# Kernel optimization log

Measured on AMD Instinct MI355X. Metric: run time of the kernel, lower is better.

The kernel has to match this reference:

```python
import jax, jax.numpy as jnp
import numpy as np

B, S, E, H = 2, 2048, 1024, 16
DH = E // H  # 64


def setup_inputs() -> dict:
    key = jax.random.key(0)
    ks = jax.random.split(key, 13)
    s = 1.0 / np.sqrt(E)
    inp = {
        'query': jax.random.normal(ks[0], (B, S, E), jnp.float32),
        'key':   jax.random.normal(ks[1], (B, S, E), jnp.float32),
        'value': jax.random.normal(ks[2], (B, S, E), jnp.float32),
        # nn.Linear weights stored [out, in]
        'Wq': jax.random.uniform(ks[3], (E, E), jnp.float32, -s, s),
        'bq': jax.random.uniform(ks[4], (E,), jnp.float32, -s, s),
        'Wk': jax.random.uniform(ks[5], (E, E), jnp.float32, -s, s),
        'bk': jax.random.uniform(ks[6], (E,), jnp.float32, -s, s),
        'Wv': jax.random.uniform(ks[7], (E, E), jnp.float32, -s, s),
        'bv': jax.random.uniform(ks[8], (E,), jnp.float32, -s, s),
        # 1x1 Conv2d over head channels: weight [H, H] (squeezed from [H,H,1,1]), bias [H]
        'Wc': jax.random.uniform(ks[9], (H, H), jnp.float32, -1.0 / np.sqrt(H), 1.0 / np.sqrt(H)),
        'bc': jax.random.uniform(ks[10], (H,), jnp.float32, -1.0 / np.sqrt(H), 1.0 / np.sqrt(H)),
        'Wo': jax.random.uniform(ks[11], (E, E), jnp.float32, -s, s),
        'bo': jax.random.uniform(ks[12], (E,), jnp.float32, -s, s),
    }
    return inp


def reference(query, key, value, Wq, bq, Wk, bk, Wv, bv, Wc, bc, Wo, bo):
    b, s = query.shape[0], query.shape[1]
    # projections -> (B, H, S, Dh)
    def split_heads(x):
        return x.reshape(b, s, H, DH).transpose(0, 2, 1, 3)
    Q = split_heads(query @ Wq.T + bq)
    K = split_heads(key @ Wk.T + bk)
    V = split_heads(value @ Wv.T + bv)
    # raw scores (B, H, S, S)
    scores = jnp.einsum('bhqd,bhkd->bhqk', Q, K) / np.sqrt(DH).astype(np.float32)
    # 1x1 conv mixes logits across heads: channel-wise matmul + bias
    noise = jnp.einsum('gh,bhqk->bgqk', Wc, scores) + bc[None, :, None, None]
    scores = scores + noise
    weights = jax.nn.softmax(scores, axis=-1)
    out = jnp.einsum('bhqk,bhkd->bhqd', weights, V)  # (B, H, S, Dh)
    out = out.transpose(0, 2, 1, 3).reshape(b, s, E)
    return out @ Wo.T + bo
```

## Files before the change

### kernel.cpp

```cpp
#include <hip/hip_runtime.h>


typedef __attribute__((ext_vector_type(8))) short bf16x8_t;
typedef __attribute__((ext_vector_type(4))) short bf16x4_t;
typedef __attribute__((ext_vector_type(4))) float f32x4_t;

__device__ inline unsigned short f2bf(float f) {
  unsigned u = __builtin_bit_cast(unsigned, f);
  u += 0x7fffu + ((u >> 16) & 1u);
  return (unsigned short)(u >> 16);
}

struct ConvArgs {
  const float* src[7];
  unsigned short* dst[7];
  int n[7];
};

__global__ __launch_bounds__(256) void convert_f32_bf16(ConvArgs a) {
  const int which = blockIdx.y;
  const int i = (blockIdx.x * 256 + threadIdx.x) * 8;
  if (i >= a.n[which]) return;
  const float* s = a.src[which] + i;
  f32x4_t x0 = *(const f32x4_t*)(s);
  f32x4_t x1 = *(const f32x4_t*)(s + 4);
  bf16x8_t o;
#pragma unroll
  for (int j = 0; j < 4; j++) o[j] = (short)f2bf(x0[j]);
#pragma unroll
  for (int j = 0; j < 4; j++) o[4 + j] = (short)f2bf(x1[j]);
  *(bf16x8_t*)(a.dst[which] + i) = o;
}

__global__ __launch_bounds__(256) void gemm_bt(
    const unsigned short* __restrict__ A, const unsigned short* __restrict__ Bt,
    const float* __restrict__ bias, void* __restrict__ C,
    int M, int N, int K, int c_is_f32)
{
  __shared__ unsigned short As[128 * 32];
  __shared__ unsigned short Bs[128 * 32];
  const int t = threadIdx.x;
  const int l = t & 63;
  const int w = t >> 6;
  const int quad = l >> 4, n16 = l & 15;
  const int wm = (w & 1) * 64, wn = (w >> 1) * 64;
  const long m0 = (long)blockIdx.x * 128, n0 = (long)blockIdx.y * 128;

  f32x4_t acc[4][4] = {};

  const unsigned short* gA = A + (m0 + (t >> 2)) * (long)K + (t & 3) * 8;
  const unsigned short* gB = Bt + (n0 + (t >> 2)) * (long)K + (t & 3) * 8;
  const long rowskip = 64l * K;

  for (int kt = 0; kt < K; kt += 32) {
    bf16x8_t ra0 = *(const bf16x8_t*)(gA + kt);
    bf16x8_t ra1 = *(const bf16x8_t*)(gA + kt + rowskip);
    bf16x8_t rb0 = *(const bf16x8_t*)(gB + kt);
    bf16x8_t rb1 = *(const bf16x8_t*)(gB + kt + rowskip);
    __syncthreads();
    *(bf16x8_t*)&As[t * 8] = ra0;
    *(bf16x8_t*)&As[2048 + t * 8] = ra1;
    *(bf16x8_t*)&Bs[t * 8] = rb0;
    *(bf16x8_t*)&Bs[2048 + t * 8] = rb1;
    __syncthreads();
    bf16x8_t af[4], bfr[4];
#pragma unroll
    for (int i = 0; i < 4; i++) {
      af[i]  = *(const bf16x8_t*)&As[(wm + i * 16 + n16) * 32 + quad * 8];
      bfr[i] = *(const bf16x8_t*)&Bs[(wn + i * 16 + n16) * 32 + quad * 8];
    }
#pragma unroll
    for (int mi = 0; mi < 4; mi++)
#pragma unroll
      for (int ni = 0; ni < 4; ni++)
        acc[mi][ni] = __builtin_amdgcn_mfma_f32_16x16x32_bf16(af[mi], bfr[ni], acc[mi][ni], 0, 0, 0);
  }

#pragma unroll
  for (int ni = 0; ni < 4; ni++) {
    const long n = n0 + wn + ni * 16 + n16;
    const float bv = bias[n];
#pragma unroll
    for (int mi = 0; mi < 4; mi++) {
#pragma unroll
      for (int r = 0; r < 4; r++) {
        const long m = m0 + wm + mi * 16 + quad * 4 + r;
        const float v = acc[mi][ni][r] + bv;
        if (c_is_f32) ((float*)C)[m * N + n] = v;
        else ((unsigned short*)C)[m * N + n] = f2bf(v);
      }
    }
  }
}

__global__ __launch_bounds__(256) void transpose_v(
    const unsigned short* __restrict__ V, unsigned short* __restrict__ VT)
{
  __shared__ unsigned short tile[64][72];
  const int t = threadIdx.x;
  const int s0 = blockIdx.x * 64, h = blockIdx.y, b = blockIdx.z;
#pragma unroll
  for (int r = 0; r < 2; r++) {
    const int elem = r * 2048 + t * 8;
    const int s = elem >> 6, d = elem & 63;
    *(bf16x8_t*)&tile[s][d] =
        *(const bf16x8_t*)&V[(size_t)(b * 2048 + s0 + s) * 1024 + h * 64 + d];
  }
  __syncthreads();
#pragma unroll
  for (int r = 0; r < 2; r++) {
    const int elem = r * 2048 + t * 8;
    const int d = elem >> 6, sl = elem & 63;
    bf16x8_t o;
#pragma unroll
    for (int j = 0; j < 8; j++) o[j] = (short)tile[sl + j][d];
    *(bf16x8_t*)&VT[((size_t)(b * 16 + h) * 64 + d) * 2048 + s0 + sl] = o;
  }
}

__global__ __launch_bounds__(1024) void attention_fused(
    const unsigned short* __restrict__ Qb, const unsigned short* __restrict__ Kb,
    const unsigned short* __restrict__ VT, const float* __restrict__ Wc,
    unsigned short* __restrict__ Obuf)
{
  __shared__ unsigned short sraw[512 * 36];
  __shared__ unsigned short pbuf2[16 * 580];
  __shared__ float alphabuf[256];
  __shared__ float lbuf[256];
  __shared__ unsigned short mmat[256];

  const int t = threadIdx.x;
  const int g = t >> 6, l = t & 63;
  const int quad = l >> 4, n16 = l & 15;

  const int id = blockIdx.x;
  const int xcd = id & 7;
  const int b = xcd >> 2;
  const int qb = (xcd & 3) * 32 + (id >> 3);
  const int q0 = qb * 16;

  if (t < 256) {
    const float v = ((((t >> 4) == (t & 15)) ? 1.0f : 0.0f) + Wc[t]) * 0.125f;
    mmat[t] = f2bf(v);
  }
  __syncthreads();

  bf16x8_t mfrag;
  if (quad < 2) mfrag = *(const bf16x8_t*)&mmat[n16 * 16 + quad * 8];
  else { bf16x8_t z = {0, 0, 0, 0, 0, 0, 0, 0}; mfrag = z; }
  const int c7 = g >> 2;

  bf16x8_t qf[2];
#pragma unroll
  for (int dr = 0; dr < 2; dr++)
    qf[dr] = *(const bf16x8_t*)&Qb[(size_t)(b * 2048 + q0 + n16) * 1024 + g * 64 + dr * 32 + quad * 8];

  const int slot = g ^ (quad << 3);
  const unsigned short* kptr = Kb + (size_t)(b * 2048 + n16) * 1024 + g * 64 + quad * 8;
  const unsigned short* vptr = VT + ((size_t)(b * 16 + g) * 64 + n16) * 2048 + quad * 8;

  bf16x8_t kf[2][2], vf[4];
  auto load_kf = [&](int kt) {
#pragma unroll
    for (int kc = 0; kc < 2; kc++)
#pragma unroll
      for (int dr = 0; dr < 2; dr++)
        kf[kc][dr] = *(const bf16x8_t*)(kptr + (size_t)(kt + kc * 16) * 1024 + dr * 32);
  };
  auto load_vf = [&](int kt) {
#pragma unroll
    for (int dc = 0; dc < 4; dc++)
      vf[dc] = *(const bf16x8_t*)(vptr + (size_t)dc * 16 * 2048 + kt);
  };
  auto qk_stage = [&]() {
    f32x4_t sf[2] = {};
#pragma unroll
    for (int kc = 0; kc < 2; kc++)
#pragma unroll
      for (int dr = 0; dr < 2; dr++)
        sf[kc] = __builtin_amdgcn_mfma_f32_16x16x32_bf16(qf[dr], kf[kc][dr], sf[kc], 0, 0, 0);
#pragma unroll
    for (int kc = 0; kc < 2; kc++)
#pragma unroll
      for (int r = 0; r < 4; r++)
        sraw[((quad * 4 + r) * 32 + kc * 16 + n16) * 36 + slot] = f2bf(sf[kc][r]);
  };

  load_kf(0);
  qk_stage();
  __syncthreads();

  f32x4_t o[4] = {};
  float m_run[4], l_run[4];
#pragma unroll
  for (int r = 0; r < 4; r++) { m_run[r] = -1e30f; l_run[r] = 0.0f; }

  for (int it = 0; it < 64; ++it) {
    const int kt = it * 32;
    load_vf(kt);
    if (it < 63) load_kf(kt + 32);

    f32x4_t mixd[2];
#pragma unroll
    for (int c2 = 0; c2 < 2; c2++) {
      const int c = g * 2 + c2;
      const unsigned short* sp = &sraw[(c * 16 + n16) * 36 + (((quad & 1) ^ c7) << 3)];
      bf16x4_t lo = *(const bf16x4_t*)sp;
      bf16x4_t hi = *(const bf16x4_t*)(sp + 4);
      bf16x8_t bb = {lo[0], lo[1], lo[2], lo[3], hi[0], hi[1], hi[2], hi[3]};
      f32x4_t z = {};
      mixd[c2] = __builtin_amdgcn_mfma_f32_16x16x32_bf16(mfrag, bb, z, 0, 0, 0);
    }

    float p0[4], p1[4], al[4];
#pragma unroll
    for (int r = 0; r < 4; r++) {
      float mx = fmaxf(mixd[0][r], mixd[1][r]);
      mx = fmaxf(mx, __shfl_xor(mx, 1));
      mx = fmaxf(mx, __shfl_xor(mx, 2));
      mx = fmaxf(mx, __shfl_xor(mx, 4));
      mx = fmaxf(mx, __shfl_xor(mx, 8));
      const float mnew = fmaxf(m_run[r], mx);
      al[r] = __expf(m_run[r] - mnew);
      m_run[r] = mnew;
      p0[r] = __expf(mixd[0][r] - mnew);
      p1[r] = __expf(mixd[1][r] - mnew);
      l_run[r] = l_run[r] * al[r] + (p0[r] + p1[r]);
    }

    const bool evn = (n16 & 1) == 0;
#pragma unroll
    for (int r = 0; r < 4; r++) {
      const float p0n = __shfl_xor(p0[r], 1);
      const float p1n = __shfl_xor(p1[r], 1);
      const float va = evn ? p0[r] : p1n;
      const float vb = evn ? p0n : p1[r];
      unsigned pk;
      asm volatile("v_cvt_pk_bf16_f32 %0, %1, %2" : "=v"(pk) : "v"(va), "v"(vb));
      const int keven = evn ? n16 : (15 + n16);
      *(unsigned*)&pbuf2[(quad * 4 + r) * 580 + g * 36 + keven] = pk;
    }
    if (n16 == 0) {
#pragma unroll
      for (int r = 0; r < 4; r++) alphabuf[(quad * 4 + r) * 16 + g] = al[r];
    }
    __syncthreads();

#pragma unroll
    for (int r = 0; r < 4; r++) {
      const float ar = alphabuf[g * 16 + quad * 4 + r];
#pragma unroll
      for (int dc = 0; dc < 4; dc++) o[dc][r] *= ar;
    }
    const unsigned short* pp = &pbuf2[g * 580 + n16 * 36 + quad * 8];
    bf16x4_t plo = *(const bf16x4_t*)pp;
    bf16x4_t phi = *(const bf16x4_t*)(pp + 4);
    bf16x8_t pf = {plo[0], plo[1], plo[2], plo[3], phi[0], phi[1], phi[2], phi[3]};
#pragma unroll
    for (int dc = 0; dc < 4; dc++)
      o[dc] = __builtin_amdgcn_mfma_f32_16x16x32_bf16(pf, vf[dc], o[dc], 0, 0, 0);

    if (it < 63) {
      qk_stage();
      __syncthreads();
    }
  }

#pragma unroll
  for (int r = 0; r < 4; r++) {
    float s = l_run[r];
    s += __shfl_xor(s, 1);
    s += __shfl_xor(s, 2);
    s += __shfl_xor(s, 4);
    s += __shfl_xor(s, 8);
    l_run[r] = s;
  }
  if (n16 == 0) {
#pragma unroll
    for (int r = 0; r < 4; r++) lbuf[(quad * 4 + r) * 16 + g] = l_run[r];
  }
  __syncthreads();
  float linv[4];
#pragma unroll
  for (int r = 0; r < 4; r++) linv[r] = 1.0f / lbuf[g * 16 + quad * 4 + r];
#pragma unroll
  for (int dc = 0; dc < 4; dc++)
#pragma unroll
    for (int r = 0; r < 4; r++) {
      const float v = o[dc][r] * linv[r];
      Obuf[(size_t)(b * 2048 + q0 + quad * 4 + r) * 1024 + g * 64 + dc * 16 + n16] = f2bf(v);
    }
}

extern "C" void kernel_launch(void* const* d_in, const int* in_sizes, int n_in,
                              void* d_out, int out_size, void* d_ws, size_t ws_size,
                              hipStream_t stream) {
  const float* query = (const float*)d_in[0];
  const float* key   = (const float*)d_in[1];
  const float* value = (const float*)d_in[2];
  const float* Wq = (const float*)d_in[3];
  const float* bq = (const float*)d_in[4];
  const float* Wk = (const float*)d_in[5];
  const float* bk = (const float*)d_in[6];
  const float* Wv = (const float*)d_in[7];
  const float* bv = (const float*)d_in[8];
  const float* Wc = (const float*)d_in[9];
  const float* Wo = (const float*)d_in[11];
  const float* bo = (const float*)d_in[12];

  char* ws = (char*)d_ws;
  const size_t MB = 1024 * 1024;
  unsigned short* q_bf  = (unsigned short*)(ws);
  unsigned short* k_bf  = (unsigned short*)(ws + 8 * MB);
  unsigned short* v_bf  = (unsigned short*)(ws + 16 * MB);
  unsigned short* wq_bf = (unsigned short*)(ws + 24 * MB);
  unsigned short* wk_bf = (unsigned short*)(ws + 26 * MB);
  unsigned short* wv_bf = (unsigned short*)(ws + 28 * MB);
  unsigned short* wo_bf = (unsigned short*)(ws + 30 * MB);
  unsigned short* Qb    = (unsigned short*)(ws + 32 * MB);
  unsigned short* Kb    = (unsigned short*)(ws + 40 * MB);
  unsigned short* Vb    = (unsigned short*)(ws + 48 * MB);
  unsigned short* VT   = k_bf;
  unsigned short* Obuf = q_bf;

  ConvArgs ca;
  ca.src[0] = query; ca.dst[0] = q_bf;  ca.n[0] = 2 * 2048 * 1024;
  ca.src[1] = key;   ca.dst[1] = k_bf;  ca.n[1] = 2 * 2048 * 1024;
  ca.src[2] = value; ca.dst[2] = v_bf;  ca.n[2] = 2 * 2048 * 1024;
  ca.src[3] = Wq;    ca.dst[3] = wq_bf; ca.n[3] = 1024 * 1024;
  ca.src[4] = Wk;    ca.dst[4] = wk_bf; ca.n[4] = 1024 * 1024;
  ca.src[5] = Wv;    ca.dst[5] = wv_bf; ca.n[5] = 1024 * 1024;
  ca.src[6] = Wo;    ca.dst[6] = wo_bf; ca.n[6] = 1024 * 1024;
  convert_f32_bf16<<<dim3(2048, 7), 256, 0, stream>>>(ca);

  gemm_bt<<<dim3(32, 8), 256, 0, stream>>>(q_bf, wq_bf, bq, Qb, 4096, 1024, 1024, 0);
  gemm_bt<<<dim3(32, 8), 256, 0, stream>>>(k_bf, wk_bf, bk, Kb, 4096, 1024, 1024, 0);
  gemm_bt<<<dim3(32, 8), 256, 0, stream>>>(v_bf, wv_bf, bv, Vb, 4096, 1024, 1024, 0);

  transpose_v<<<dim3(32, 16, 2), 256, 0, stream>>>(Vb, VT);

  attention_fused<<<dim3(256), 1024, 0, stream>>>(Qb, Kb, VT, Wc, Obuf);

  gemm_bt<<<dim3(32, 8), 256, 0, stream>>>(Obuf, wo_bf, bo, d_out, 4096, 1024, 1024, 1);
}
```

Measured before the change: 479.4 us.

## Split attention over two key halves and merge partial softmax results

Splits the key sequence into two halves so the attention kernel launches twice as many blocks (512 instead of 256). Each block writes unnormalized fp32 partial outputs plus its running max and sum, and a new merge kernel combines the halves. The change also switches to exp2 with a log2e-folded scale, transposes the head-mix MFMA so each lane holds one row's max, and moves the next K prefetch after the barrier. The cost is extra fp32 partial traffic, one more kernel launch, and reuse of d_out as scratch space.

New measurement: 671.4 us. 1.4x slower.

```diff
diff --git a/kernel.cpp b/kernel.cpp
--- a/kernel.cpp
+++ b/kernel.cpp
@@ -118,15 +118,15 @@
   }
 }
 
-__global__ __launch_bounds__(1024) void attention_fused(
+__global__ __launch_bounds__(1024, 8) void attention_fused(
     const unsigned short* __restrict__ Qb, const unsigned short* __restrict__ Kb,
     const unsigned short* __restrict__ VT, const float* __restrict__ Wc,
-    unsigned short* __restrict__ Obuf)
+    float* __restrict__ Op0, float* __restrict__ Op1,
+    float* __restrict__ Mm, float* __restrict__ Ll)
 {
   __shared__ unsigned short sraw[512 * 36];
   __shared__ unsigned short pbuf2[16 * 580];
-  __shared__ float alphabuf[256];
-  __shared__ float lbuf[256];
+  __shared__ float alphabuf[16 * 17];
   __shared__ unsigned short mmat[256];
 
   const int t = threadIdx.x;
@@ -136,11 +136,15 @@
   const int id = blockIdx.x;
   const int xcd = id & 7;
   const int b = xcd >> 2;
-  const int qb = (xcd & 3) * 32 + (id >> 3);
+  const int rem = id >> 3;
+  const int kb = rem & 1;
+  const int qb = (xcd & 3) * 32 + (rem >> 1);
   const int q0 = qb * 16;
-
+  const int k0 = kb * 1024;
+
+  for (int i = t; i < 512 * 36; i += 1024) sraw[i] = 0;
   if (t < 256) {
-    const float v = ((((t >> 4) == (t & 15)) ? 1.0f : 0.0f) + Wc[t]) * 0.125f;
+    const float v = ((((t >> 4) == (t & 15)) ? 1.0f : 0.0f) + Wc[t]) * 0.1803368801111204f;
     mmat[t] = f2bf(v);
   }
   __syncthreads();
@@ -156,8 +160,8 @@
     qf[dr] = *(const bf16x8_t*)&Qb[(size_t)(b * 2048 + q0 + n16) * 1024 + g * 64 + dr * 32 + quad * 8];
 
   const int slot = g ^ (quad << 3);
-  const unsigned short* kptr = Kb + (size_t)(b * 2048 + n16) * 1024 + g * 64 + quad * 8;
-  const unsigned short* vptr = VT + ((size_t)(b * 16 + g) * 64 + n16) * 2048 + quad * 8;
+  const unsigned short* kptr = Kb + (size_t)(b * 2048 + k0 + n16) * 1024 + g * 64 + quad * 8;
+  const unsigned short* vptr = VT + ((size_t)(b * 16 + g) * 64 + n16) * 2048 + k0 + quad * 8;
 
   bf16x8_t kf[2][2], vf[4];
   auto load_kf = [&](int kt) {
@@ -191,64 +195,60 @@
   __syncthreads();
 
   f32x4_t o[4] = {};
-  float m_run[4], l_run[4];
-#pragma unroll
-  for (int r = 0; r < 4; r++) { m_run[r] = -1e30f; l_run[r] = 0.0f; }
-
-  for (int it = 0; it < 64; ++it) {
+  float m_run = -1e30f, l_run = 0.0f;
+
+  for (int it = 0; it < 32; ++it) {
     const int kt = it * 32;
     load_vf(kt);
-    if (it < 63) load_kf(kt + 32);
 
     f32x4_t mixd[2];
 #pragma unroll
     for (int c2 = 0; c2 < 2; c2++) {
       const int c = g * 2 + c2;
-      const unsigned short* sp = &sraw[(c * 16 + n16) * 36 + (((quad & 1) ^ c7) << 3)];
+      const unsigned short* sp = &sraw[(c * 16 + n16) * 36 + ((quad ^ c7) << 3)];
       bf16x4_t lo = *(const bf16x4_t*)sp;
       bf16x4_t hi = *(const bf16x4_t*)(sp + 4);
-      bf16x8_t bb = {lo[0], lo[1], lo[2], lo[3], hi[0], hi[1], hi[2], hi[3]};
+      bf16x8_t aa = {lo[0], lo[1], lo[2], lo[3], hi[0], hi[1], hi[2], hi[3]};
       f32x4_t z = {};
-      mixd[c2] = __builtin_amdgcn_mfma_f32_16x16x32_bf16(mfrag, bb, z, 0, 0, 0);
-    }
-
-    float p0[4], p1[4], al[4];
+      mixd[c2] = __builtin_amdgcn_mfma_f32_16x16x32_bf16(aa, mfrag, z, 0, 0, 0);
+    }
+
+    float mx = fmaxf(fmaxf(fmaxf(mixd[0][0], mixd[0][1]), fmaxf(mixd[0][2], mixd[0][3])),
+                     fmaxf(fmaxf(mixd[1][0], mixd[1][1]), fmaxf(mixd[1][2], mixd[1][3])));
+    mx = fmaxf(mx, __shfl_xor(mx, 16));
+    mx = fmaxf(mx, __shfl_xor(mx, 32));
+    const float mnew = fmaxf(m_run, mx);
+    const float alpha = exp2f(m_run - mnew);
+    m_run = mnew;
+    float p[2][4];
+    float lsum = 0.0f;
+#pragma unroll
+    for (int c2 = 0; c2 < 2; c2++)
+#pragma unroll
+      for (int r = 0; r < 4; r++) {
+        p[c2][r] = exp2f(mixd[c2][r] - mnew);
+        lsum += p[c2][r];
+      }
+    l_run = l_run * alpha + lsum;
+
+    const int pbase = n16 * 580 + g * 36 + quad * 4;
+#pragma unroll
+    for (int c2 = 0; c2 < 2; c2++)
+#pragma unroll
+      for (int rp = 0; rp < 2; rp++) {
+        unsigned pk;
+        asm volatile("v_cvt_pk_bf16_f32 %0, %1, %2"
+                     : "=v"(pk) : "v"(p[c2][2 * rp]), "v"(p[c2][2 * rp + 1]));
+        *(unsigned*)&pbuf2[pbase + c2 * 16 + 2 * rp] = pk;
+      }
+    if (quad == 0) alphabuf[n16 * 17 + g] = alpha;
+    __syncthreads();
+
+    if (it < 31) load_kf(kt + 32);
+
 #pragma unroll
     for (int r = 0; r < 4; r++) {
-      float mx = fmaxf(mixd[0][r], mixd[1][r]);
-      mx = fmaxf(mx, __shfl_xor(mx, 1));
-      mx = fmaxf(mx, __shfl_xor(mx, 2));
-      mx = fmaxf(mx, __shfl_xor(mx, 4));
-      mx = fmaxf(mx, __shfl_xor(mx, 8));
-      const float mnew = fmaxf(m_run[r], mx);
-      al[r] = __expf(m_run[r] - mnew);
-      m_run[r] = mnew;
-      p0[r] = __expf(mixd[0][r] - mnew);
-      p1[r] = __expf(mixd[1][r] - mnew);
-      l_run[r] = l_run[r] * al[r] + (p0[r] + p1[r]);
-    }
-
-    const bool evn = (n16 & 1) == 0;
-#pragma unroll
-    for (int r = 0; r < 4; r++) {
-      const float p0n = __shfl_xor(p0[r], 1);
-      const float p1n = __shfl_xor(p1[r], 1);
-      const float va = evn ? p0[r] : p1n;
-      const float vb = evn ? p0n : p1[r];
-      unsigned pk;
-      asm volatile("v_cvt_pk_bf16_f32 %0, %1, %2" : "=v"(pk) : "v"(va), "v"(vb));
-      const int keven = evn ? n16 : (15 + n16);
-      *(unsigned*)&pbuf2[(quad * 4 + r) * 580 + g * 36 + keven] = pk;
-    }
-    if (n16 == 0) {
-#pragma unroll
-      for (int r = 0; r < 4; r++) alphabuf[(quad * 4 + r) * 16 + g] = al[r];
-    }
-    __syncthreads();
-
-#pragma unroll
-    for (int r = 0; r < 4; r++) {
-      const float ar = alphabuf[g * 16 + quad * 4 + r];
+      const float ar = alphabuf[g * 17 + quad * 4 + r];
 #pragma unroll
       for (int dc = 0; dc < 4; dc++) o[dc][r] *= ar;
     }
@@ -260,36 +260,56 @@
     for (int dc = 0; dc < 4; dc++)
       o[dc] = __builtin_amdgcn_mfma_f32_16x16x32_bf16(pf, vf[dc], o[dc], 0, 0, 0);
 
-    if (it < 63) {
+    if (it < 31) {
       qk_stage();
       __syncthreads();
     }
   }
 
-#pragma unroll
-  for (int r = 0; r < 4; r++) {
-    float s = l_run[r];
-    s += __shfl_xor(s, 1);
-    s += __shfl_xor(s, 2);
-    s += __shfl_xor(s, 4);
-    s += __shfl_xor(s, 8);
-    l_run[r] = s;
-  }
-  if (n16 == 0) {
-#pragma unroll
-    for (int r = 0; r < 4; r++) lbuf[(quad * 4 + r) * 16 + g] = l_run[r];
-  }
-  __syncthreads();
-  float linv[4];
-#pragma unroll
-  for (int r = 0; r < 4; r++) linv[r] = 1.0f / lbuf[g * 16 + quad * 4 + r];
+  l_run += __shfl_xor(l_run, 16);
+  l_run += __shfl_xor(l_run, 32);
+  if (quad == 0) {
+    const size_t mi = ((size_t)(kb * 2 + b) * 16 + n16) * 2048 + q0 + g;
+    Mm[mi] = m_run;
+    Ll[mi] = l_run;
+  }
+  float* const ob = kb ? Op1 : Op0;
 #pragma unroll
   for (int dc = 0; dc < 4; dc++)
 #pragma unroll
-    for (int r = 0; r < 4; r++) {
-      const float v = o[dc][r] * linv[r];
-      Obuf[(size_t)(b * 2048 + q0 + quad * 4 + r) * 1024 + g * 64 + dc * 16 + n16] = f2bf(v);
-    }
+    for (int r = 0; r < 4; r++)
+      ob[((size_t)(b * 2048 + q0 + quad * 4 + r)) * 1024 + g * 64 + dc * 16 + n16] = o[dc][r];
+}
+
+__global__ __launch_bounds__(256) void merge_halves(
+    const float* __restrict__ Op0, const float* __restrict__ Op1,
+    const float* __restrict__ Mm, const float* __restrict__ Ll,
+    unsigned short* __restrict__ Obuf)
+{
+  const int i = blockIdx.x * 256 + threadIdx.x;
+  const size_t e8 = (size_t)i * 8;
+  const int e = (int)(e8 & 1023);
+  const int q = (int)((e8 >> 10) & 2047);
+  const int b = (int)(e8 >> 21);
+  const int h = e >> 6;
+  const size_t row = (size_t)b * 2048 + q;
+  const size_t mi = ((size_t)b * 16 + h) * 2048 + q;
+  const float m0 = Mm[mi], m1 = Mm[2 * 16 * 2048 + mi];
+  const float l0 = Ll[mi], l1 = Ll[2 * 16 * 2048 + mi];
+  const float m = fmaxf(m0, m1);
+  const float w0 = exp2f(m0 - m), w1 = exp2f(m1 - m);
+  const float inv = 1.0f / (l0 * w0 + l1 * w1);
+  const float s0 = w0 * inv, s1 = w1 * inv;
+  const float* pa = Op0 + row * 1024 + e;
+  const float* pb = Op1 + row * 1024 + e;
+  f32x4_t a0 = *(const f32x4_t*)pa, a1 = *(const f32x4_t*)(pa + 4);
+  f32x4_t b0 = *(const f32x4_t*)pb, b1 = *(const f32x4_t*)(pb + 4);
+  bf16x8_t o8;
+#pragma unroll
+  for (int j = 0; j < 4; j++) o8[j] = (short)f2bf(a0[j] * s0 + b0[j] * s1);
+#pragma unroll
+  for (int j = 0; j < 4; j++) o8[4 + j] = (short)f2bf(a1[j] * s0 + b1[j] * s1);
+  *(bf16x8_t*)&Obuf[row * 1024 + e] = o8;
 }
 
 extern "C" void kernel_launch(void* const* d_in, const int* in_sizes, int n_in,
@@ -320,6 +340,10 @@
   unsigned short* Qb    = (unsigned short*)(ws + 32 * MB);
   unsigned short* Kb    = (unsigned short*)(ws + 40 * MB);
   unsigned short* Vb    = (unsigned short*)(ws + 48 * MB);
+  float* Op0 = (float*)(ws + 56 * MB);
+  float* Mm  = (float*)(ws + 72 * MB);
+  float* Ll  = (float*)(ws + 72 * MB + 512 * 1024);
+  float* Op1 = (float*)d_out;
   unsigned short* VT   = k_bf;
   unsigned short* Obuf = q_bf;
 
@@ -339,7 +363,9 @@
 
   transpose_v<<<dim3(32, 16, 2), 256, 0, stream>>>(Vb, VT);
 
-  attention_fused<<<dim3(256), 1024, 0, stream>>>(Qb, Kb, VT, Wc, Obuf);
+  attention_fused<<<dim3(512), 1024, 0, stream>>>(Qb, Kb, VT, Wc, Op0, Op1, Mm, Ll);
+
+  merge_halves<<<dim3(2048), 256, 0, stream>>>(Op0, Op1, Mm, Ll, Obuf);
 
   gemm_bt<<<dim3(32, 8), 256, 0, stream>>>(Obuf, wo_bf, bo, d_out, 4096, 1024, 1024, 1);
 }
```
